# Performance work log

Hardware: AMD Instinct MI355X
Metric: run time of the kernel (lower is better)

## Reference

```python
import jax, jax.numpy as jnp
import numpy as np

T_STEPS = 4000          # T_ms / dt = 1000 / 0.25
N_IN, N_OUT = 64, 10
HID = [1024, 1024]
DT, TAU = 0.25, 10.0
BETA = float(np.exp(-DT / TAU))   # beta_snn
THR = 1.0                          # thr_snn
SLOPE = 1.0                        # spike_snn uses slope=1.0
W_STD = 32.0                       # W_STD_CUBA

@jax.custom_vjp
def spike(u):
    # SurrogateSpike.forward: heaviside on (mem - thr)
    return (u >= 0).astype(u.dtype)

def _spike_fwd(u):
    return spike(u), u

def _spike_bwd(u, g):
    # fast-sigmoid surrogate: slope / (1 + slope*|u|)^2
    grad = SLOPE / (1.0 + SLOPE * jnp.abs(u)) ** 2
    return (g * grad,)

spike.defvjp(_spike_fwd, _spike_bwd)

def setup_inputs() -> dict:
    key = jax.random.key(0)
    ks = jax.random.split(key, 8)
    B = 16
    # Bernoulli(0.05) input spike train, time-major [T, B, N_IN]
    input_spikes = (jax.random.uniform(ks[0], (T_STEPS, B, N_IN)) < 0.05).astype(jnp.float32)
    sizes = [N_IN] + HID + [N_OUT]
    inp = {"input_spikes": input_spikes}
    for i, (n_pre, n_post) in enumerate(zip(sizes[:-1], sizes[1:])):
        # init_weight 'normal': clamp(N(0, W_STD), min=0) / n_pre
        w = jnp.maximum(jax.random.normal(ks[i + 1], (n_pre, n_post)) * W_STD, 0.0) / n_pre
        inp[f"W{i}"] = w.astype(jnp.float32)
        inp[f"b{i}"] = jnp.zeros((n_post,), jnp.float32)
    return inp

def reference(input_spikes, W0, b0, W1, b1, W2, b2):
    # Dale's law: feedforward weights clamped >= 0 in forward
    Ws = [jnp.maximum(W, 0.0) for W in (W0, W1, W2)]
    bs = [b0, b1, b2]
    B = input_spikes.shape[1]
    sizes = HID + [N_OUT]
    mems0 = tuple(jnp.zeros((B, n), input_spikes.dtype) for n in sizes)

    def step(mems, s_in):
        s = s_in
        new_mems = []
        for l in range(len(Ws)):
            I = s @ Ws[l] + bs[l]                 # [B, n_post]
            m = BETA * mems[l] + I                # LIF decay + drive
            sp = spike(m - THR)                   # surrogate-grad spike
            m = jnp.where(sp > 0, 0.0, m)         # hard reset to zero
            new_mems.append(m)
            s = sp
        return tuple(new_mems), s                 # emit output-layer spikes

    _, out_spikes = jax.lax.scan(step, mems0, input_spikes)
    return out_spikes  # [T, B, N_OUT]
```

## Files before the change

### kernel.cpp

```cpp
#include <hip/hip_runtime.h>
#include <hip/hip_bf16.h>
#include <math.h>


#define T_STEPS 4000
#define NB 16
#define N_IN 64
#define NH 1024
#define N_OUT 10
#define SEGO 40
#define SEGH 40

typedef __attribute__((ext_vector_type(8))) short bf16x8;
typedef __attribute__((ext_vector_type(4))) float f32x4;
typedef __hip_bfloat16 bf16;
typedef unsigned long long u64;

#define ASG(p) (const __attribute__((address_space(1))) void*)(p)
#define ASL(p) (__attribute__((address_space(3))) void*)(p)

#define BETA_C 0.97530991202833261687f


__global__ __launch_bounds__(256) void k_prep(
    const float* __restrict__ in_sp, u64* __restrict__ mask,
    const float* __restrict__ W1, bf16* __restrict__ BT1,
    const float* __restrict__ W2, bf16* __restrict__ BT2,
    float* __restrict__ mst, int nM, int ZB, int MB) {
    __shared__ float Wlds[64][65];
    int b = blockIdx.x;
    const int tid = threadIdx.x;
    if (b < ZB) {
        int i = b * 256 + tid;
        if (i < nM) mst[i] = 0.f;
        return;
    }
    b -= ZB;
    if (b < MB) {
        int w = b * 4 + (tid >> 6);
        int lane = tid & 63;
        float v = in_sp[(size_t)w * 64 + lane];
        u64 bal = __ballot(v > 0.5f);
        if (lane == 0) mask[w] = bal;
        return;
    }
    b -= MB;
    if (b < 256) {
        const int lane = tid & 63;
        const int wr   = tid >> 6;
        const int k0 = (b & 15) * 64;
        const int n0 = (b >> 4) * 64;
#pragma unroll
        for (int rr = 0; rr < 16; ++rr) {
            int kl = wr * 16 + rr;
            Wlds[kl][lane] = W1[(size_t)(k0 + kl) * 1024 + n0 + lane];
        }
        __syncthreads();
#pragma unroll
        for (int rr = 0; rr < 16; ++rr) {
            int nl = wr * 16 + rr;
            float w = fmaxf(Wlds[lane][nl], 0.f);
            bf16 h = __float2bfloat16(w);
            float hf = __bfloat162float(h);
            bf16 l = __float2bfloat16(w - hf);
            size_t base = (size_t)(n0 + nl) * 2048 + 2 * k0 + lane;
            BT1[base] = h;
            BT1[base + 64] = l;
        }
        return;
    }
    b -= 256;
    {
        int idx = b * 256 + tid;
        int total = 128 * 2 * NH;
        if (idx >= total) return;
        int n  = idx / (2 * NH);
        int k2 = idx - n * (2 * NH);
        int lo = (k2 >= NH);
        int k = lo ? (k2 - NH) : k2;
        float v = 0.f;
        if (n < N_OUT) {
            float w = fmaxf(W2[(size_t)k * N_OUT + n], 0.f);
            float hi = __bfloat162float(__float2bfloat16(w));
            v = lo ? (w - hi) : w;
        }
        BT2[idx] = __float2bfloat16(v);
    }
}

__global__ void k_unpack(const u64* __restrict__ BITS, float* __restrict__ out,
                         int total) {
    int idx = blockIdx.x * 256 + threadIdx.x;
    if (idx >= total) return;
    int t   = idx / (NB * N_OUT);
    int rem = idx - t * (NB * N_OUT);
    int b = rem / N_OUT;
    int k = rem - b * N_OUT;
    u64 w = BITS[(size_t)(t / SEGO) * 256 + b * 16 + k];
    out[idx] = ((w >> (t % SEGO)) & 1ULL) ? 1.f : 0.f;
}


__device__ __forceinline__ void scan_out_body(
    const float* __restrict__ I2, const float* __restrict__ bias,
    float* __restrict__ mstate, u64* __restrict__ BITS,
    int Tc, float* seg, int tid) {
    float* segA = seg;
    float* segB = seg + SEGO * 256;
    const bool act = tid < 256;
    const int lane = tid & 63;
    const int wave = tid >> 6;
    const int k = tid & 15;
    float m = 0.f, bj = 0.f;
    if (act) {
        m = mstate[tid];
        bj = (k < N_OUT) ? bias[k] : 0.f;
    }
    const int nseg = Tc / SEGO;

#define O_PREFETCH(SEGBUF, SIDX)                                            \
    if (act) {                                                              \
        const float* src = I2 + (size_t)(SIDX) * SEGO * 256                 \
                              + (size_t)wave * 256 + lane * 4;              \
        _Pragma("unroll")                                                   \
        for (int g = 0; g < SEGO / 4; ++g)                                  \
            __builtin_amdgcn_global_load_lds(                               \
                ASG(src + (size_t)(g * 4) * 256),                           \
                ASL(&SEGBUF[(g * 4 + wave) * 256]), 16, 0, 0);              \
    }

#define O_PROC(SEGBUF, SIDX)                                                \
    if (act) {                                                              \
        u64 obits = 0;                                                      \
        _Pragma("unroll")                                                   \
        for (int sb = 0; sb < SEGO / 8; ++sb) {                             \
            float v[8];                                                     \
            _Pragma("unroll")                                               \
            for (int u = 0; u < 8; ++u)                                     \
                v[u] = SEGBUF[(sb * 8 + u) * 256 + tid];                    \
            _Pragma("unroll")                                               \
            for (int u = 0; u < 8; ++u) {                                   \
                m = fmaf(BETA_C, m, v[u] + bj);                             \
                bool sp = (m >= 1.0f);                                      \
                obits |= ((u64)(sp ? 1 : 0)) << (sb * 8 + u);               \
                m = sp ? 0.f : m;                                           \
            }                                                               \
        }                                                                   \
        BITS[(size_t)(SIDX) * 256 + tid] = obits;                           \
    }

    O_PREFETCH(segA, 0);
    O_PREFETCH(segB, 1);
    asm volatile("s_waitcnt vmcnt(10)" ::: "memory");
    __builtin_amdgcn_sched_barrier(0);
    __builtin_amdgcn_s_barrier();
    for (int s = 0; s < nseg; s += 2) {
        O_PROC(segA, s);
        if (s + 2 < nseg) {
            O_PREFETCH(segA, s + 2);
            asm volatile("s_waitcnt vmcnt(11)" ::: "memory");
        } else {
            asm volatile("s_waitcnt vmcnt(1)" ::: "memory");
        }
        __builtin_amdgcn_sched_barrier(0);
        __builtin_amdgcn_s_barrier();
        O_PROC(segB, s + 1);
        if (s + 3 < nseg) {
            O_PREFETCH(segB, s + 3);
            asm volatile("s_waitcnt vmcnt(11)" ::: "memory");
            __builtin_amdgcn_sched_barrier(0);
            __builtin_amdgcn_s_barrier();
        } else if (s + 2 < nseg) {
            asm volatile("s_waitcnt vmcnt(1)" ::: "memory");
            __builtin_amdgcn_sched_barrier(0);
            __builtin_amdgcn_s_barrier();
        }
    }
    if (act) mstate[tid] = m;
#undef O_PREFETCH
#undef O_PROC
}

__global__ __launch_bounds__(256) void k_scan_out(
    const float* __restrict__ I2, const float* __restrict__ bias,
    float* __restrict__ mstate, u64* __restrict__ BITS, int Tc) {
    __shared__ __align__(16) float seg[2 * SEGO * 256];
    scan_out_body(I2, bias, mstate, BITS, Tc, seg, threadIdx.x);
}


__device__ __forceinline__ void scan_l0_body(
    const u64* __restrict__ mask, const float* __restrict__ W0,
    const float* __restrict__ bias, float* __restrict__ mstate,
    bf16* __restrict__ S, int Tc, int b0, int lane, float* IL) {
    const int b  = b0 >> 4;
    const int q  = b0 & 15;
    const int j0 = q * 64;
    const int gid = b0 * 64 + lane;
    const int r16 = lane & 15;
    const int kg  = lane >> 4;
    bf16x8 bh[4][2], bl[4][2];
#pragma unroll
    for (int jt = 0; jt < 4; ++jt)
#pragma unroll
        for (int kk = 0; kk < 2; ++kk)
#pragma unroll
            for (int e = 0; e < 8; ++e) {
                int k = kk * 32 + kg * 8 + e;
                float w = fmaxf(W0[(size_t)k * 1024 + j0 + jt * 16 + r16], 0.f);
                bf16 h = __float2bfloat16(w);
                float hf = __bfloat162float(h);
                bf16 l = __float2bfloat16(w - hf);
                bh[jt][kk][e] = *(short*)&h;
                bl[jt][kk][e] = *(short*)&l;
            }
    float m = mstate[gid];
    const float bj = bias[j0 + lane];
    const size_t stride = (size_t)NB * NH;
    const int ntile = Tc / 16;
    const int tmax = ntile - 1;

#define LOADM(TT) mask[(size_t)(((TT) <= tmax ? (TT) : tmax) * 16 + r16) * NB + b]

#define L0_COMPUTE(MSK, P)                                                  \
    {                                                                       \
        f32x4 acc[4] = {};                                                  \
        _Pragma("unroll")                                                   \
        for (int kk = 0; kk < 2; ++kk) {                                    \
            unsigned byte8 = (unsigned)(((MSK) >> (kk * 32 + kg * 8)) & 0xFF); \
            bf16x8 af;                                                      \
            _Pragma("unroll")                                               \
            for (int e = 0; e < 8; ++e)                                     \
                af[e] = ((byte8 >> e) & 1) ? (short)0x3F80 : (short)0;      \
            _Pragma("unroll")                                               \
            for (int jt = 0; jt < 4; ++jt) {                                \
                acc[jt] = __builtin_amdgcn_mfma_f32_16x16x32_bf16(          \
                    af, bh[jt][kk], acc[jt], 0, 0, 0);                      \
                acc[jt] = __builtin_amdgcn_mfma_f32_16x16x32_bf16(          \
                    af, bl[jt][kk], acc[jt], 0, 0, 0);                      \
            }                                                               \
        }                                                                   \
        _Pragma("unroll")                                                   \
        for (int jt = 0; jt < 4; ++jt)                                      \
            _Pragma("unroll")                                               \
            for (int rr = 0; rr < 4; ++rr)                                  \
                IL[(P) * 1088 + (kg * 4 + rr) * 68 + jt * 16 + r16] = acc[jt][rr]; \
    }

    u64 mc = LOADM(0);
    L0_COMPUTE(mc, 0);
    u64 mn = LOADM(1);
    for (int tt = 0; tt < ntile; ++tt) {
        __builtin_amdgcn_s_barrier();
        float v[16];
#pragma unroll
        for (int u = 0; u < 16; ++u)
            v[u] = IL[(tt & 1) * 1088 + u * 68 + lane];
        u64 m2 = LOADM(tt + 2);
        if (tt + 1 < ntile) L0_COMPUTE(mn, (tt + 1) & 1);
        unsigned short o[16];
#pragma unroll
        for (int u = 0; u < 16; ++u) {
            m = fmaf(BETA_C, m, v[u] + bj);
            bool sp = (m >= 1.0f);
            o[u] = sp ? (unsigned short)0x3F80 : (unsigned short)0;
            m = sp ? 0.f : m;
        }
#pragma unroll
        for (int u = 0; u < 16; ++u)
            ((unsigned short*)S)[(size_t)(tt * 16 + u) * stride + gid] = o[u];
        mn = m2;
    }
    mstate[gid] = m;
#undef L0_COMPUTE
#undef LOADM
}

__global__ __launch_bounds__(64) void k_scan_l0(
    const u64* __restrict__ mask, const float* __restrict__ W0,
    const float* __restrict__ bias, float* __restrict__ mstate,
    bf16* __restrict__ S, int Tc) {
    __shared__ __align__(16) float IL[2 * 16 * 68];
    scan_l0_body(mask, W0, bias, mstate, S, Tc, blockIdx.x, threadIdx.x, IL);
}


__global__ __launch_bounds__(256) void k_gemm_thin(
    const bf16* __restrict__ A, const bf16* __restrict__ BT,
    float* __restrict__ C) {
    const int tid  = threadIdx.x;
    const int lane = tid & 63;
    const int wave = tid >> 6;
    const int r16 = lane & 15;
    const int kg  = lane >> 4;
    const int m0 = blockIdx.x * 64 + wave * 16;
    f32x4 acc = {};
    const bf16* ap = A + (size_t)(m0 + r16) * 1024 + kg * 8;
    const bf16* bh = BT + (size_t)r16 * 2048 + kg * 8;
    const bf16* bl = bh + 1024;
#pragma unroll 8
    for (int kt = 0; kt < 32; ++kt) {
        const int ka = kt * 32;
        bf16x8 af  = *(const bf16x8*)(ap + ka);
        bf16x8 bfh = *(const bf16x8*)(bh + ka);
        bf16x8 bfl = *(const bf16x8*)(bl + ka);
        acc = __builtin_amdgcn_mfma_f32_16x16x32_bf16(af, bfh, acc, 0, 0, 0);
        acc = __builtin_amdgcn_mfma_f32_16x16x32_bf16(af, bfl, acc, 0, 0, 0);
    }
#pragma unroll
    for (int rr = 0; rr < 4; ++rr)
        C[(size_t)(m0 + kg * 4 + rr) * 16 + r16] = acc[rr];
}


__global__ __launch_bounds__(512) void k_gemm8(
    const bf16* __restrict__ A, const bf16* __restrict__ BT,
    float* __restrict__ C, int gx,
    const float* __restrict__ I2t, const float* __restrict__ b2t,
    float* __restrict__ m2t, u64* __restrict__ BITSt, int tcT, int doTailOut,
    const u64* __restrict__ maskN, const float* __restrict__ W0N,
    const float* __restrict__ b0N, float* __restrict__ m0N,
    bf16* __restrict__ SN, int nL0blk) {
    __shared__ __align__(16) char LDS[131072];
    const int tid  = threadIdx.x;
    const int lane = tid & 63;
    const int wave = tid >> 6;

    const int nwg = gridDim.x - doTailOut - nL0blk;
    const int wg  = blockIdx.x;
    if (wg >= nwg) {
        int tix = wg - nwg;
        if (tix < doTailOut) {
            scan_out_body(I2t, b2t, m2t, BITSt, tcT, (float*)LDS, tid);
        } else {
            int unit = (tix - doTailOut) * 8 + wave;
            float* IL = (float*)LDS + wave * 2176;
            scan_l0_body(maskN, W0N, b0N, m0N, SN, tcT, unit, lane, IL);
        }
        return;
    }

    const int KA = 1024;
    const int q = nwg >> 3, r = nwg & 7;
    const int xcd = wg & 7, idx0 = wg >> 3;
    const int swz = (xcd < r ? xcd * (q + 1) : r * (q + 1) + (xcd - r) * q) + idx0;
    const int gy = nwg / gx;
    const int n0 = (swz % gy) * 256;
    const int m0 = (swz / gy) * 256;

    const int wm = (wave >> 2) * 128;
    const int wn = (wave & 3) * 64;
    const int r16l = lane & 15;
    const int kg   = lane >> 4;
    const int hA   = wave >> 2;
    const int hB   = (wave & 3) >> 1;
    const int wn64 = wave & 1;

    const int po = (r16l * 64 + kg * 16) ^ (((r16l >> 3) & 1) << 5);
    const char* bA[2] = { LDS + hA * 16384 + po,
                          LDS + 32768 + hA * 16384 + po };
    const char* bB[2] = { LDS + 65536 + hB * 16384 + po,
                          LDS + 98304 + hB * 16384 + po };
    const int bOff = wn64 * 8192;

    int s_row[2], s_col[2];
#pragma unroll
    for (int rr = 0; rr < 2; ++rr) {
        int d = (rr * 512 + tid) * 16;
        int l = d ^ (((d >> 9) & 1) << 5);
        int sub = l >> 10;
        int w = l & 1023;
        s_row[rr] = (sub >> 1) * 16 + (w >> 6);
        s_col[rr] = ((sub & 1) * 64 + (w & 63)) >> 1;
    }

#define STAGE_A(ADST, HALF, K0)                                             \
    {                                                                       \
        _Pragma("unroll")                                                   \
        for (int rr = 0; rr < 2; ++rr)                                      \
            __builtin_amdgcn_global_load_lds(                               \
                ASG(A + (size_t)(m0 + (HALF) * 128 + s_row[rr]) * KA        \
                    + (K0) + s_col[rr]),                                    \
                ASL(LDS + (ADST) * 32768 + (HALF) * 16384                   \
                    + (rr * 512 + wave * 64) * 16),                         \
                16, 0, 0);                                                  \
    }
#define STAGE_B(BUF, HALF, K0)                                              \
    {                                                                       \
        _Pragma("unroll")                                                   \
        for (int rr = 0; rr < 2; ++rr)                                      \
            __builtin_amdgcn_global_load_lds(                               \
                ASG(BT + (size_t)(n0 + (HALF) * 128 + s_row[rr]) * 2048     \
                    + (K0) + s_col[rr]),                                    \
                ASL(LDS + 65536 + (BUF) * 32768 + (HALF) * 16384            \
                    + (rr * 512 + wave * 64) * 16),                         \
                16, 0, 0);                                                  \
    }

    f32x4 acc[8][4] = {};
    bf16x8 a[4][2], b[4][2];

#define MM(MIB, NIB)                                                        \
    {                                                                       \
        _Pragma("unroll")                                                   \
        for (int i = 0; i < 4; ++i)                                         \
            _Pragma("unroll")                                               \
            for (int j = 0; j < 2; ++j) {                                   \
                acc[(MIB) + i][(NIB) + j] =                                 \
                    __builtin_amdgcn_mfma_f32_16x16x32_bf16(                \
                        a[i][0], b[(NIB) + j][0], acc[(MIB) + i][(NIB) + j], 0, 0, 0); \
                acc[(MIB) + i][(NIB) + j] =                                 \
                    __builtin_amdgcn_mfma_f32_16x16x32_bf16(                \
                        a[i][1], b[(NIB) + j][1], acc[(MIB) + i][(NIB) + j], 0, 0, 0); \
            }                                                               \
    }

#define PH_SYNC()                                                           \
    __builtin_amdgcn_s_barrier();                                           \
    asm volatile("s_waitcnt lgkmcnt(0)" ::: "memory");                      \
    __builtin_amdgcn_sched_barrier(0);

#define KT_EVEN(ABUF, BKN, AKN)                                             \
    {                                                                       \
        _Pragma("unroll")                                                   \
        for (int i = 0; i < 4; ++i) {                                       \
            a[i][0] = *(const bf16x8*)(bA[ABUF] + i * 2048);                \
            a[i][1] = *(const bf16x8*)(bA[ABUF] + i * 2048 + 1024);         \
        }                                                                   \
        _Pragma("unroll")                                                   \
        for (int j = 0; j < 2; ++j) {                                       \
            b[j][0] = *(const bf16x8*)(bB[0] + bOff + j * 2048);            \
            b[j][1] = *(const bf16x8*)(bB[0] + bOff + j * 2048 + 1024);     \
        }                                                                   \
        PH_SYNC();                                                          \
        __builtin_amdgcn_s_setprio(1);                                      \
        MM(0, 0);                                                           \
        __builtin_amdgcn_s_setprio(0);                                      \
        __builtin_amdgcn_s_barrier();                                       \
        _Pragma("unroll")                                                   \
        for (int j = 0; j < 2; ++j) {                                       \
            b[2 + j][0] = *(const bf16x8*)(bB[0] + bOff + (2 + j) * 2048);  \
            b[2 + j][1] = *(const bf16x8*)(bB[0] + bOff + (2 + j) * 2048 + 1024); \
        }                                                                   \
        PH_SYNC();                                                          \
        __builtin_amdgcn_s_setprio(1);                                      \
        MM(0, 2);                                                           \
        __builtin_amdgcn_s_setprio(0);                                      \
        __builtin_amdgcn_s_barrier();                                       \
        _Pragma("unroll")                                                   \
        for (int i = 0; i < 4; ++i) {                                       \
            a[i][0] = *(const bf16x8*)(bA[ABUF] + (4 + i) * 2048);          \
            a[i][1] = *(const bf16x8*)(bA[ABUF] + (4 + i) * 2048 + 1024);   \
        }                                                                   \
        STAGE_B(0, 0, BKN);                                                 \
        STAGE_B(0, 1, BKN);                                                 \
        PH_SYNC();                                                          \
        __builtin_amdgcn_s_setprio(1);                                      \
        MM(4, 0);                                                           \
        __builtin_amdgcn_s_setprio(0);                                      \
        __builtin_amdgcn_s_barrier();                                       \
        STAGE_A((ABUF) ^ 1, 0, AKN);                                        \
        STAGE_A((ABUF) ^ 1, 1, AKN);                                        \
        PH_SYNC();                                                          \
        __builtin_amdgcn_s_setprio(1);                                      \
        MM(4, 2);                                                           \
        __builtin_amdgcn_s_setprio(0);                                      \
        asm volatile("s_waitcnt vmcnt(8)" ::: "memory");                    \
        __builtin_amdgcn_sched_barrier(0);                                  \
        __builtin_amdgcn_s_barrier();                                       \
    }

#define KT_ODD(ABUF, BKN)                                                   \
    {                                                                       \
        _Pragma("unroll")                                                   \
        for (int i = 0; i < 4; ++i) {                                       \
            a[i][0] = *(const bf16x8*)(bA[ABUF] + i * 2048);                \
            a[i][1] = *(const bf16x8*)(bA[ABUF] + i * 2048 + 1024);         \
        }                                                                   \
        _Pragma("unroll")                                                   \
        for (int j = 0; j < 2; ++j) {                                       \
            b[j][0] = *(const bf16x8*)(bB[1] + bOff + j * 2048);            \
            b[j][1] = *(const bf16x8*)(bB[1] + bOff + j * 2048 + 1024);     \
        }                                                                   \
        PH_SYNC();                                                          \
        __builtin_amdgcn_s_setprio(1);                                      \
        MM(0, 0);                                                           \
        __builtin_amdgcn_s_setprio(0);                                      \
        __builtin_amdgcn_s_barrier();                                       \
        _Pragma("unroll")                                                   \
        for (int j = 0; j < 2; ++j) {                                       \
            b[2 + j][0] = *(const bf16x8*)(bB[1] + bOff + (2 + j) * 2048);  \
            b[2 + j][1] = *(const bf16x8*)(bB[1] + bOff + (2 + j) * 2048 + 1024); \
        }                                                                   \
        PH_SYNC();                                                          \
        __builtin_amdgcn_s_setprio(1);                                      \
        MM(0, 2);                                                           \
        __builtin_amdgcn_s_setprio(0);                                      \
        __builtin_amdgcn_s_barrier();                                       \
        _Pragma("unroll")                                                   \
        for (int i = 0; i < 4; ++i) {                                       \
            a[i][0] = *(const bf16x8*)(bA[ABUF] + (4 + i) * 2048);          \
            a[i][1] = *(const bf16x8*)(bA[ABUF] + (4 + i) * 2048 + 1024);   \
        }                                                                   \
        STAGE_B(1, 0, BKN);                                                 \
        STAGE_B(1, 1, BKN);                                                 \
        PH_SYNC();                                                          \
        __builtin_amdgcn_s_setprio(1);                                      \
        MM(4, 0);                                                           \
        __builtin_amdgcn_s_setprio(0);                                      \
        __builtin_amdgcn_s_barrier();                                       \
        PH_SYNC();                                                          \
        __builtin_amdgcn_s_setprio(1);                                      \
        MM(4, 2);                                                           \
        __builtin_amdgcn_s_setprio(0);                                      \
        asm volatile("s_waitcnt vmcnt(4)" ::: "memory");                    \
        __builtin_amdgcn_sched_barrier(0);                                  \
        __builtin_amdgcn_s_barrier();                                       \
    }

    STAGE_B(0, 0, 0);  STAGE_B(0, 1, 0);
    STAGE_A(0, 0, 0);  STAGE_A(0, 1, 0);
    STAGE_B(1, 0, 64); STAGE_B(1, 1, 64);
    asm volatile("s_waitcnt vmcnt(4)" ::: "memory");
    __builtin_amdgcn_sched_barrier(0);
    __builtin_amdgcn_s_barrier();

    for (int it2 = 0; it2 < 16; it2 += 2) {
        const int ak1 = (64 * (it2 + 1)) & 1023;
        const int be1 = (128 * (it2 + 1)) & 2047;
        KT_EVEN(0, be1, ak1);
        KT_ODD(0, be1 + 64);
        const int ak2 = (64 * (it2 + 2)) & 1023;
        const int be2 = (128 * (it2 + 2)) & 2047;
        KT_EVEN(1, be2, ak2);
        KT_ODD(1, be2 + 64);
    }
    asm volatile("s_waitcnt vmcnt(0)" ::: "memory");
    __builtin_amdgcn_sched_barrier(0);

#pragma unroll
    for (int mi = 0; mi < 8; ++mi)
#pragma unroll
        for (int ni = 0; ni < 4; ++ni)
#pragma unroll
            for (int rr = 0; rr < 4; ++rr) {
                int row = m0 + wm + mi * 16 + kg * 4 + rr;
                int col = n0 + wn + ni * 16 + r16l;
                C[(size_t)row * 1024 + col] = acc[mi][ni][rr];
            }
#undef KT_ODD
#undef KT_EVEN
#undef PH_SYNC
#undef MM
#undef STAGE_A
#undef STAGE_B
}


__global__ __launch_bounds__(64) void k_scan_hidden(
    const float* __restrict__ I, const float* __restrict__ bias,
    float* __restrict__ mstate, bf16* __restrict__ S, int Tc, float beta) {
    __shared__ __align__(16) float segA[SEGH * 64];
    __shared__ __align__(16) float segB[SEGH * 64];
    const int lane = threadIdx.x;
    const int gid  = blockIdx.x * 64 + lane;
    const int j = gid & (NH - 1);
    float m = mstate[gid];
    const float bj = bias[j];
    const size_t stride = (size_t)NB * NH;
    const int nseg = Tc / SEGH;
    const int lrow = lane >> 4;
    const int lcol = (lane & 15) << 2;

#define H_PREFETCH(SEGBUF, SIDX)                                            \
    {                                                                       \
        const float* src = I + (size_t)(SIDX) * SEGH * stride               \
                             + (size_t)lrow * stride + blockIdx.x * 64 + lcol; \
        _Pragma("unroll")                                                   \
        for (int g = 0; g < SEGH / 4; ++g)                                  \
            __builtin_amdgcn_global_load_lds(                               \
                ASG(src + (size_t)(g * 4) * stride),                        \
                ASL(&SEGBUF[g * 256]), 16, 0, 0);                           \
    }

#define H_PROC(SEGBUF, SIDX)                                                \
    {                                                                       \
        const int btt = (SIDX) * SEGH;                                      \
        _Pragma("unroll")                                                   \
        for (int sb = 0; sb < SEGH / 8; ++sb) {                             \
            float v[8];                                                     \
            _Pragma("unroll")                                               \
            for (int u = 0; u < 8; ++u)                                     \
                v[u] = SEGBUF[(sb * 8 + u) * 64 + lane];                    \
            unsigned short o[8];                                            \
            _Pragma("unroll")                                               \
            for (int u = 0; u < 8; ++u) {                                   \
                m = fmaf(beta, m, v[u] + bj);                               \
                bool sp = (m >= 1.0f);                                      \
                o[u] = sp ? (unsigned short)0x3F80 : (unsigned short)0;     \
                m = sp ? 0.f : m;                                           \
            }                                                               \
            _Pragma("unroll")                                               \
            for (int u = 0; u < 8; ++u)                                     \
                ((unsigned short*)S)[(size_t)(btt + sb * 8 + u) * stride + gid] = o[u]; \
        }                                                                   \
    }

    H_PREFETCH(segA, 0);
    H_PREFETCH(segB, 1);
    asm volatile("s_waitcnt vmcnt(10)" ::: "memory");
    __builtin_amdgcn_sched_barrier(0);
    for (int s = 0; s < nseg; s += 2) {
        H_PROC(segA, s);
        if (s + 2 < nseg) {
            H_PREFETCH(segA, s + 2);
            asm volatile("s_waitcnt vmcnt(50)" ::: "memory");
        } else {
            asm volatile("s_waitcnt vmcnt(40)" ::: "memory");
        }
        __builtin_amdgcn_sched_barrier(0);
        H_PROC(segB, s + 1);
        if (s + 3 < nseg) {
            H_PREFETCH(segB, s + 3);
            asm volatile("s_waitcnt vmcnt(50)" ::: "memory");
            __builtin_amdgcn_sched_barrier(0);
        } else if (s + 2 < nseg) {
            asm volatile("s_waitcnt vmcnt(40)" ::: "memory");
            __builtin_amdgcn_sched_barrier(0);
        }
    }
    mstate[gid] = m;
#undef H_PREFETCH
#undef H_PROC
}


extern "C" void kernel_launch(void* const* d_in, const int* in_sizes, int n_in,
                              void* d_out, int out_size, void* d_ws, size_t ws_size,
                              hipStream_t stream) {
    const float* in_sp = (const float*)d_in[0];
    const float* W0 = (const float*)d_in[1];
    const float* b0 = (const float*)d_in[2];
    const float* W1 = (const float*)d_in[3];
    const float* b1 = (const float*)d_in[4];
    const float* W2 = (const float*)d_in[5];
    const float* b2 = (const float*)d_in[6];
    float* out = (float*)d_out;

    char* p = (char*)d_ws;
    auto carve = [&](size_t bytes) -> void* {
        char* r = p; p += (bytes + 255) & ~(size_t)255; return (void*)r;
    };
    u64*  MASK  = (u64*)carve((size_t)T_STEPS * NB * 8);
    bf16* BT1   = (bf16*)carve((size_t)NH * 2 * NH * 2);
    bf16* BT2   = (bf16*)carve((size_t)128 * 2 * NH * 2);
    float* m0s  = (float*)carve((size_t)NB * NH * 4);
    float* m1s  = (float*)carve((size_t)NB * NH * 4);
    float* m2s  = (float*)carve((size_t)NB * 16 * 4);
    float* I2BUF = (float*)carve((size_t)T_STEPS * NB * 16 * 4);
    u64*  BITS  = (u64*)carve((size_t)(T_STEPS / SEGO) * 256 * 8);
    size_t fixed = (size_t)(p - (char*)d_ws);

    const int tc_opts[3] = {2000, 800, 400};
    int Tc = 400;
    for (int i = 0; i < 3; ++i) {
        size_t Mc_ = (size_t)tc_opts[i] * NB;
        size_t need = fixed
            + ((Mc_ * NH * 4 + 255) & ~(size_t)255)
            + ((Mc_ * NH * 2 + 255) & ~(size_t)255);
        if (need <= ws_size) { Tc = tc_opts[i]; break; }
    }
    size_t Mc = (size_t)Tc * NB;
    float* IBUF = (float*)carve(Mc * NH * 4);
    bf16*  S0   = (bf16*)carve(Mc * NH * 2);
    size_t sbytes = (Mc * NH * 2 + 255) & ~(size_t)255;
    int sdbuf = ((size_t)(p - (char*)d_ws) + sbytes <= ws_size) ? 1 : 0;
    bf16* S1 = sdbuf ? (bf16*)carve(Mc * NH * 2) : S0;
    auto Sb = [&](int c) -> bf16* { return (c & 1) ? S1 : S0; };

    int nM = NB * NH * 2 + NB * 16;
    const int ZB = (nM + 255) / 256;
    const int MB = (T_STEPS * NB) / 4;
    const int L2B = (128 * 2 * NH + 255) / 256;
    k_prep<<<ZB + MB + 256 + L2B, 256, 0, stream>>>(
        in_sp, MASK, W1, BT1, W2, BT2, m0s, nM, ZB, MB);

    const int C = T_STEPS / Tc;
    const int gx8 = (int)(Mc / 256);
    const int gthin = (int)(Mc / 64);

    k_scan_l0<<<256, 64, 0, stream>>>(MASK, W0, b0, m0s, Sb(0), Tc);

    const float beta = (float)exp(-0.25 / 10.0);
    for (int c = 0; c < C; ++c) {
        int t0 = c * Tc;
        int doOut = (c >= 1) ? 1 : 0;
        int nL0   = (sdbuf && c + 1 < C) ? 32 : 0;
        int tp = (c - 1) * Tc;
        k_gemm8<<<gx8 * 4 + doOut + nL0, 512, 0, stream>>>(
            Sb(c), BT1, IBUF, gx8,
            doOut ? I2BUF + (size_t)tp * NB * 16 : nullptr, b2, m2s,
            doOut ? BITS + (size_t)(tp / SEGO) * 256 : nullptr, Tc, doOut,
            nL0 ? MASK + (size_t)(t0 + Tc) * NB : nullptr, W0, b0, m0s,
            nL0 ? Sb(c + 1) : nullptr, nL0);
        k_scan_hidden<<<(NB * NH) / 64, 64, 0, stream>>>(IBUF, b1, m1s, Sb(c), Tc, beta);
        k_gemm_thin<<<gthin, 256, 0, stream>>>(Sb(c), BT2,
                                               I2BUF + (size_t)t0 * NB * 16);
        if (!sdbuf && c + 1 < C)
            k_scan_l0<<<256, 64, 0, stream>>>(MASK + (size_t)(t0 + Tc) * NB,
                                              W0, b0, m0s, Sb(c + 1), Tc);
    }
    int tl = (C - 1) * Tc;
    k_scan_out<<<1, 256, 0, stream>>>(I2BUF + (size_t)tl * NB * 16, b2, m2s,
                                      BITS + (size_t)(tl / SEGO) * 256, Tc);
    int nOut = T_STEPS * NB * N_OUT;
    k_unpack<<<(nOut + 255) / 256, 256, 0, stream>>>(BITS, out, nOut);
}
```

Baseline: 657.9 us.

## Deepen hidden-scan prefetch ring and stage spike output through LDS for wide stores

Result: slower. 675.9 us (+2.7%).

```diff
diff --git a/kernel.cpp b/kernel.cpp
--- a/kernel.cpp
+++ b/kernel.cpp
@@ -12,6 +12,7 @@
 #define SEGH 40
 
 typedef __attribute__((ext_vector_type(8))) short bf16x8;
+typedef __attribute__((ext_vector_type(8))) unsigned short u16x8;
 typedef __attribute__((ext_vector_type(4))) float f32x4;
 typedef __hip_bfloat16 bf16;
 typedef unsigned long long u64;
@@ -560,8 +561,8 @@
 __global__ __launch_bounds__(64) void k_scan_hidden(
     const float* __restrict__ I, const float* __restrict__ bias,
     float* __restrict__ mstate, bf16* __restrict__ S, int Tc, float beta) {
-    __shared__ __align__(16) float segA[SEGH * 64];
-    __shared__ __align__(16) float segB[SEGH * 64];
+    __shared__ __align__(16) float seg4[4 * SEGH * 64];
+    __shared__ __align__(16) unsigned short OST[SEGH * 64];
     const int lane = threadIdx.x;
     const int gid  = blockIdx.x * 64 + lane;
     const int j = gid & (NH - 1);
@@ -571,67 +572,68 @@
     const int nseg = Tc / SEGH;
     const int lrow = lane >> 4;
     const int lcol = (lane & 15) << 2;
-
-#define H_PREFETCH(SEGBUF, SIDX)                                            \
+    unsigned short* Sp = (unsigned short*)S + blockIdx.x * 64;
+
+#define H_PRE(SIDX)                                                         \
     {                                                                       \
         const float* src = I + (size_t)(SIDX) * SEGH * stride               \
                              + (size_t)lrow * stride + blockIdx.x * 64 + lcol; \
+        float* dst = seg4 + ((SIDX) & 3) * (SEGH * 64);                     \
         _Pragma("unroll")                                                   \
         for (int g = 0; g < SEGH / 4; ++g)                                  \
             __builtin_amdgcn_global_load_lds(                               \
                 ASG(src + (size_t)(g * 4) * stride),                        \
-                ASL(&SEGBUF[g * 256]), 16, 0, 0);                           \
-    }
-
-#define H_PROC(SEGBUF, SIDX)                                                \
+                ASL(dst + g * 256), 16, 0, 0);                              \
+    }
+
+#define H_PROC(SIDX)                                                        \
     {                                                                       \
+        const float* sb = seg4 + ((SIDX) & 3) * (SEGH * 64);                \
         const int btt = (SIDX) * SEGH;                                      \
         _Pragma("unroll")                                                   \
-        for (int sb = 0; sb < SEGH / 8; ++sb) {                             \
+        for (int q8 = 0; q8 < SEGH / 8; ++q8) {                             \
             float v[8];                                                     \
             _Pragma("unroll")                                               \
             for (int u = 0; u < 8; ++u)                                     \
-                v[u] = SEGBUF[(sb * 8 + u) * 64 + lane];                    \
-            unsigned short o[8];                                            \
+                v[u] = sb[(q8 * 8 + u) * 64 + lane];                        \
             _Pragma("unroll")                                               \
             for (int u = 0; u < 8; ++u) {                                   \
                 m = fmaf(beta, m, v[u] + bj);                               \
                 bool sp = (m >= 1.0f);                                      \
-                o[u] = sp ? (unsigned short)0x3F80 : (unsigned short)0;     \
+                OST[(q8 * 8 + u) * 64 + lane] =                             \
+                    sp ? (unsigned short)0x3F80 : (unsigned short)0;        \
                 m = sp ? 0.f : m;                                           \
             }                                                               \
-            _Pragma("unroll")                                               \
-            for (int u = 0; u < 8; ++u)                                     \
-                ((unsigned short*)S)[(size_t)(btt + sb * 8 + u) * stride + gid] = o[u]; \
-        }                                                                   \
-    }
-
-    H_PREFETCH(segA, 0);
-    H_PREFETCH(segB, 1);
-    asm volatile("s_waitcnt vmcnt(10)" ::: "memory");
-    __builtin_amdgcn_sched_barrier(0);
-    for (int s = 0; s < nseg; s += 2) {
-        H_PROC(segA, s);
-        if (s + 2 < nseg) {
-            H_PREFETCH(segA, s + 2);
-            asm volatile("s_waitcnt vmcnt(50)" ::: "memory");
-        } else {
-            asm volatile("s_waitcnt vmcnt(40)" ::: "memory");
-        }
-        __builtin_amdgcn_sched_barrier(0);
-        H_PROC(segB, s + 1);
-        if (s + 3 < nseg) {
-            H_PREFETCH(segB, s + 3);
-            asm volatile("s_waitcnt vmcnt(50)" ::: "memory");
-            __builtin_amdgcn_sched_barrier(0);
-        } else if (s + 2 < nseg) {
-            asm volatile("s_waitcnt vmcnt(40)" ::: "memory");
-            __builtin_amdgcn_sched_barrier(0);
-        }
-    }
+        }                                                                   \
+        asm volatile("s_waitcnt lgkmcnt(0)" ::: "memory");                  \
+        __builtin_amdgcn_sched_barrier(0);                                  \
+        _Pragma("unroll")                                                   \
+        for (int g = 0; g < SEGH / 8; ++g) {                                \
+            int rrow = g * 8 + (lane >> 3);                                 \
+            u16x8 val = *(const u16x8*)&OST[rrow * 64 + (lane & 7) * 8];    \
+            *(u16x8*)&Sp[(size_t)(btt + rrow) * stride + (lane & 7) * 8] = val; \
+        }                                                                   \
+    }
+
+#define HW(N) asm volatile("s_waitcnt vmcnt(" #N ")" ::: "memory");         \
+              __builtin_amdgcn_sched_barrier(0);
+
+    H_PRE(0); H_PRE(1); H_PRE(2);
+    HW(20); H_PRE(3); H_PROC(0);
+    HW(25); H_PRE(4); H_PROC(1);
+    HW(30); H_PRE(5); H_PROC(2);
+    for (int s = 3; s < nseg - 2; ++s) {
+        HW(35);
+        if (s + 3 < nseg) H_PRE(s + 3);
+        H_PROC(s);
+    }
+    HW(25); H_PROC(nseg - 2);
+    HW(15); H_PROC(nseg - 1);
+
     mstate[gid] = m;
-#undef H_PREFETCH
+#undef HW
 #undef H_PROC
+#undef H_PRE
 }
 
 
```
